# Kernel tuning notes

Hardware: AMD Instinct MI355X
Metric: run time of the kernel (lower is better)

## Reference

```python
import jax, jax.numpy as jnp
import numpy as np

NGF = 64
EPS = 1e-5


def _rpad(x):
    # ReflectionPad2d(1)
    return jnp.pad(x, ((0, 0), (0, 0), (1, 1), (1, 1)), mode='reflect')


def _inorm(x):
    # InstanceNorm2d(affine=False): per-sample, per-channel over H,W
    m = x.mean(axis=(2, 3), keepdims=True)
    v = ((x - m) ** 2).mean(axis=(2, 3), keepdims=True)
    return (x - m) / jnp.sqrt(v + EPS)


def _pac_conv(xp, gp, w, b):
    # Pixel-adaptive conv (pac.PacConv2d, kernel_type='gaussian', k=3, pad=0).
    # xp: (B,C,H+2,W+2) padded input; gp: (B,Cg,H+2,W+2) padded guide;
    # w: (O,C,3,3), b: (O,)
    B, C, Hp, Wp = xp.shape
    H, W = Hp - 2, Wp - 2
    gc = gp[:, :, 1:1 + H, 1:1 + W]  # guide value at each output pixel (patch center)
    out = jnp.zeros((B, w.shape[0], H, W), xp.dtype)
    for ky in range(3):
        for kx in range(3):
            gs = gp[:, :, ky:ky + H, kx:kx + W]
            # Gaussian adaptive kernel: exp(-0.5 * ||g_nb - g_center||^2), summed over guide channels
            k = jnp.exp(-0.5 * jnp.sum((gs - gc) ** 2, axis=1, keepdims=True))  # (B,1,H,W)
            xs = xp[:, :, ky:ky + H, kx:kx + W] * k
            out = out + jnp.einsum('oc,bchw->bohw', w[:, :, ky, kx], xs)
    return out + b[None, :, None, None]


def _pa_resblock(h, guide, wa, ba, wb, bb):
    gp = _rpad(guide)
    t = h
    h = _pac_conv(_rpad(h), gp, wa, ba)
    h = jax.nn.relu(_inorm(h))
    h = _pac_conv(_rpad(h), gp, wb, bb)
    h = _inorm(h)
    return t + h


def setup_inputs() -> dict:
    key = jax.random.key(0)
    ks = jax.random.split(key, 20)
    B, Cin, H, W = 4, 1, 256, 256
    d = {
        'x': jax.random.normal(ks[0], (B, Cin, H, W), jnp.float32),
        'grad_img': jax.random.normal(ks[1], (B, Cin, H, W), jnp.float32),
        'w0': jax.random.normal(ks[2], (NGF, Cin, 1, 1), jnp.float32) * 0.5,
        'b0': jnp.zeros((NGF,), jnp.float32),
        'wf': jax.random.normal(ks[3], (NGF, NGF, 3, 3), jnp.float32) * 0.05,
        'bf': jnp.zeros((NGF,), jnp.float32),
    }
    for i in (1, 2, 3):
        d[f'w{i}a'] = jax.random.normal(ks[3 + 2 * i], (NGF, NGF, 3, 3), jnp.float32) * 0.05
        d[f'b{i}a'] = jnp.zeros((NGF,), jnp.float32)
        d[f'w{i}b'] = jax.random.normal(ks[4 + 2 * i], (NGF, NGF, 3, 3), jnp.float32) * 0.05
        d[f'b{i}b'] = jnp.zeros((NGF,), jnp.float32)
    return d


def reference(x, grad_img, w0, b0, wf, bf,
              w1a, b1a, w1b, b1b,
              w2a, b2a, w2b, b2b,
              w3a, b3a, w3b, b3b):
    # type == 'ir': y = minmax(grad_img) is computed but unused; guide = x
    guide = x
    # 1x1 stem conv
    h = jnp.einsum('oc,bchw->bohw', w0[:, :, 0, 0], x) + b0[None, :, None, None]
    h = jax.nn.relu(_pa_resblock(h, guide, w1a, b1a, w1b, b1b))
    h = jax.nn.relu(_pa_resblock(h, guide, w2a, b2a, w2b, b2b))
    h = jax.nn.relu(_pa_resblock(h, guide, w3a, b3a, w3b, b3b))
    # model2: reflect pad + 3x3 conv + relu
    hp = _rpad(h)
    out = jax.lax.conv_general_dilated(
        hp, wf, window_strides=(1, 1), padding='VALID',
        dimension_numbers=('NCHW', 'OIHW', 'NCHW'))
    out = jax.nn.relu(out + bf[None, :, None, None])
    return out
```

## Files before the change

### kernel.cpp

```cpp
#include <hip/hip_runtime.h>
#include <hip/hip_bf16.h>
#include <math.h>

#define BN 4
#define CHN 64
#define HH 256
#define WW 256
#define HWSZ (HH*WW)
#define EPSV 1e-5f
#define CP 72

typedef __attribute__((ext_vector_type(8)))  short  short8;
typedef __attribute__((ext_vector_type(4)))  short  short4v;
typedef __attribute__((ext_vector_type(16))) float  floatx16;

__device__ __forceinline__ int refl(int i, int n){ if(i<0)i=-i; if(i>=n)i=2*n-2-i; return i; }
__device__ __forceinline__ short f2bf(float f){ __hip_bfloat16 h=__float2bfloat16(f); return __builtin_bit_cast(short,h); }
__device__ __forceinline__ float bf2f(short s){ unsigned u=((unsigned)(unsigned short)s)<<16; return __builtin_bit_cast(float,u); }

__global__ void guide_kernel(const float* __restrict__ x, float* __restrict__ Kb) {
    int idx = blockIdx.x * 256 + threadIdx.x;
    if (idx >= BN*HWSZ) return;
    int b = idx / HWSZ, p = idx - b*HWSZ;
    int y = p / WW, xx = p - y*WW;
    const float* g = x + b*HWSZ;
    float gc = g[p];
#pragma unroll
    for (int t = 0; t < 9; ++t) {
        int yy  = refl(y + t/3 - 1, HH);
        int xx2 = refl(xx + t%3 - 1, WW);
        float d = g[yy*WW + xx2] - gc;
        Kb[(b*9 + t)*HWSZ + p] = __expf(-0.5f*d*d);
    }
}

__global__ void pack_all(const float* w1,const float* w2,const float* w3,const float* w4,
                         const float* w5,const float* w6,const float* w7, short* __restrict__ Ap){
    const float* wsrc[7] = {w1,w2,w3,w4,w5,w6,w7};
    int layer = blockIdx.y;
    int tid = blockIdx.x*256 + threadIdx.x;
    int j    = tid & 7;
    int lane = (tid >> 3) & 63;
    int frag = tid >> 9;
    int oh = frag & 1, cg = (frag >> 1) & 3, t = frag >> 3;
    int o = oh*32 + (lane & 31);
    int c = cg*16 + (lane >> 5)*8 + j;
    Ap[(size_t)layer*36864 + tid] = f2bf(wsrc[layer][(o*CHN + c)*9 + t]);
}

__global__ void conv1x1_kernel(const float* __restrict__ x, const float* __restrict__ w0,
                               const float* __restrict__ b0, short* __restrict__ A){
    int idx = blockIdx.x*256 + threadIdx.x;
    int oc = idx & 7;
    int px = (idx >> 3) % HWSZ;
    int b  = idx / (HWSZ*8);
    float xv = x[(size_t)b*HWSZ + px];
    short8 r;
#pragma unroll
    for (int j = 0; j < 8; ++j) {
        int c = oc*8 + j;
        r[j] = f2bf(fmaf(w0[c], xv, b0[c]));
    }
    *(short8*)(A + ((size_t)(b*HWSZ + px))*64 + oc*8) = r;
}

__global__ void zero_stats(float* st){
    int idx = blockIdx.x*256 + threadIdx.x;
    if (idx < 6*BN*64*2) st[idx] = 0.f;
}

template<int NORM, int HASK, int FINAL>
__global__ void __launch_bounds__(256, 4) pac_mfma(
    const short* __restrict__ hin, const float* __restrict__ Kb,
    const short* __restrict__ Ap, const float* __restrict__ bias,
    const float* __restrict__ stin, short* __restrict__ outb, float* __restrict__ outf)
{
    __shared__ short lds[4*34*CP];

    int b  = blockIdx.z;
    int y0 = blockIdx.y * 2;
    int x0 = blockIdx.x * 32;
    int tid = threadIdx.x, lane = tid & 63, wave = tid >> 6;
    int ln2 = lane & 31, hi = lane >> 5, oh = wave & 1, wrow = wave >> 1;
    const short* hb = hin + (size_t)b*HWSZ*64;
    const float* stb = stin + b*64*2;

    float mean[8], rstd[8];
    if (NORM) {
        int c0 = (tid & 7) * 8;
#pragma unroll
        for (int j = 0; j < 8; ++j) {
            float s = stb[(c0+j)*2], s2 = stb[(c0+j)*2+1];
            float m = s * (1.f/HWSZ);
            float var = s2 * (1.f/HWSZ) - m*m;
            mean[j] = m; rstd[j] = rsqrtf(fmaxf(var, 0.f) + EPSV);
        }
    }
#pragma unroll
    for (int it = 0; it < 4; ++it) {
        int chunk = tid + it*256;
        int r = chunk >> 8, o = chunk & 255, px = o >> 3, oc = o & 7;
        int yy = refl(y0 - 1 + r, HH);
        short8 v = *(const short8*)(hb + ((size_t)(yy*WW + x0 + px))*64 + oc*8);
        if (NORM) {
#pragma unroll
            for (int j = 0; j < 8; ++j) {
                float f = bf2f(v[j]);
                f = fmaxf((f - mean[j]) * rstd[j], 0.f);
                v[j] = f2bf(f);
            }
        }
        *(short8*)(lds + (r*34 + 1 + px)*CP + oc*8) = v;
    }
    {
        int r = tid >> 6, c = tid & 63;
        int xm = (x0 == 0) ? 1 : x0 - 1;
        int xp = (x0 + 32 == WW) ? WW - 2 : x0 + 32;
        int yy = refl(y0 - 1 + r, HH);
        float fa = bf2f(hb[((size_t)(yy*WW + xm))*64 + c]);
        float fb = bf2f(hb[((size_t)(yy*WW + xp))*64 + c]);
        if (NORM) {
            float s = stb[c*2], s2 = stb[c*2+1];
            float m = s * (1.f/HWSZ);
            float rs = rsqrtf(fmaxf(s2*(1.f/HWSZ) - m*m, 0.f) + EPSV);
            fa = fmaxf((fa - m)*rs, 0.f);
            fb = fmaxf((fb - m)*rs, 0.f);
        }
        lds[(r*34 + 0)*CP + c]  = f2bf(fa);
        lds[(r*34 + 33)*CP + c] = f2bf(fb);
    }
    __syncthreads();

    float kv[9];
    if (HASK) {
#pragma unroll
        for (int t = 0; t < 9; ++t)
            kv[t] = Kb[((size_t)(b*9 + t))*HWSZ + (y0 + wrow)*WW + x0 + ln2];
    }

    floatx16 acc = (floatx16)(0.f);
    const short8* Ap8 = (const short8*)Ap;
#pragma unroll
    for (int t = 0; t < 9; ++t) {
        int dy = t/3 - 1, dx = t%3 - 1;
        int rr = wrow + dy + 1;
        floatx16 tmp;
#pragma unroll
        for (int cg = 0; cg < 4; ++cg) {
            short8 bf = *(const short8*)(lds + (rr*34 + 1 + ln2 + dx)*CP + cg*16 + hi*8);
            short8 af = Ap8[((size_t)(t*4 + cg)*2 + oh)*64 + lane];
            if (HASK)
                tmp = __builtin_amdgcn_mfma_f32_32x32x16_bf16(af, bf, cg == 0 ? (floatx16)(0.f) : tmp, 0, 0, 0);
            else
                acc = __builtin_amdgcn_mfma_f32_32x32x16_bf16(af, bf, acc, 0, 0, 0);
        }
        if (HASK) {
#pragma unroll
            for (int r = 0; r < 16; ++r) acc[r] = fmaf(kv[t], tmp[r], acc[r]);
        }
    }

    int y = y0 + wrow, x = x0 + ln2;
#pragma unroll
    for (int q = 0; q < 4; ++q) {
        int o0 = oh*32 + hi*4 + 8*q;
        float4 bq = *(const float4*)(bias + o0);
        if (FINAL) {
#pragma unroll
            for (int jj = 0; jj < 4; ++jj) {
                float val = acc[q*4 + jj] + ((float*)&bq)[jj];
                val = fmaxf(val, 0.f);
                outf[((size_t)(b*64 + o0 + jj))*HWSZ + y*WW + x] = val;
            }
        } else {
            short4v pk;
#pragma unroll
            for (int jj = 0; jj < 4; ++jj) pk[jj] = f2bf(acc[q*4 + jj] + ((float*)&bq)[jj]);
            *(short4v*)(outb + ((size_t)b*HWSZ + (size_t)(y*WW + x))*64 + o0) = pk;
        }
    }
}

__global__ void __launch_bounds__(256) stats_k(const short* __restrict__ t, float* __restrict__ st){
    int b = blockIdx.y, chunk = blockIdx.x;
    int tid = threadIdx.x, oc = tid & 7, pxl = tid >> 3;
    const short* tb = t + (size_t)b*HWSZ*64;
    float s[8] = {0}, s2[8] = {0};
    for (int i = 0; i < 64; ++i) {
        int px = chunk*2048 + i*32 + pxl;
        short8 v = *(const short8*)(tb + (size_t)px*64 + oc*8);
#pragma unroll
        for (int j = 0; j < 8; ++j) { float f = bf2f(v[j]); s[j] += f; s2[j] += f*f; }
    }
#pragma unroll
    for (int mask = 8; mask <= 32; mask <<= 1) {
#pragma unroll
        for (int j = 0; j < 8; ++j) { s[j] += __shfl_xor(s[j], mask); s2[j] += __shfl_xor(s2[j], mask); }
    }
    __shared__ float sm[4][8][16];
    int lane = tid & 63, wave = tid >> 6;
    if (lane < 8) {
#pragma unroll
        for (int j = 0; j < 8; ++j) { sm[wave][lane][j] = s[j]; sm[wave][lane][8+j] = s2[j]; }
    }
    __syncthreads();
    if (tid < 8) {
#pragma unroll
        for (int j = 0; j < 8; ++j) {
            float a = 0, bsq = 0;
#pragma unroll
            for (int w = 0; w < 4; ++w) { a += sm[w][tid][j]; bsq += sm[w][tid][8+j]; }
            atomicAdd(&st[(b*64 + tid*8 + j)*2],     a);
            atomicAdd(&st[(b*64 + tid*8 + j)*2 + 1], bsq);
        }
    }
}

__global__ void addnorm_relu(short* __restrict__ A, const short* __restrict__ C,
                             const float* __restrict__ st){
    int idx = blockIdx.x*256 + threadIdx.x;
    int oc = idx & 7;
    size_t pq = (size_t)(idx >> 3);
    int b = (int)(pq / HWSZ);
    size_t base = pq*64 + oc*8;
    short8 a = *(short8*)(A + base);
    short8 c = *(const short8*)(C + base);
#pragma unroll
    for (int j = 0; j < 8; ++j) {
        int cc = oc*8 + j;
        float s = st[(b*64+cc)*2], s2 = st[(b*64+cc)*2+1];
        float m = s * (1.f/HWSZ);
        float rs = rsqrtf(fmaxf(s2*(1.f/HWSZ) - m*m, 0.f) + EPSV);
        float f = bf2f(a[j]) + (bf2f(c[j]) - m)*rs;
        a[j] = f2bf(fmaxf(f, 0.f));
    }
    *(short8*)(A + base) = a;
}

extern "C" void kernel_launch(void* const* d_in, const int* in_sizes, int n_in,
                              void* d_out, int out_size, void* d_ws, size_t ws_size,
                              hipStream_t stream) {
    const float* x   = (const float*)d_in[0];
    const float* w0  = (const float*)d_in[2];
    const float* b0  = (const float*)d_in[3];
    const float* wf  = (const float*)d_in[4];
    const float* bf  = (const float*)d_in[5];
    const float* w1a = (const float*)d_in[6];  const float* b1a = (const float*)d_in[7];
    const float* w1b = (const float*)d_in[8];  const float* b1b = (const float*)d_in[9];
    const float* w2a = (const float*)d_in[10]; const float* b2a = (const float*)d_in[11];
    const float* w2b = (const float*)d_in[12]; const float* b2b = (const float*)d_in[13];
    const float* w3a = (const float*)d_in[14]; const float* b3a = (const float*)d_in[15];
    const float* w3b = (const float*)d_in[16]; const float* b3b = (const float*)d_in[17];

    float* ws   = (float*)d_ws;
    float* Kb   = ws;
    short* A    = (short*)(Kb + (size_t)BN*9*HWSZ);
    short* Bb   = A + (size_t)BN*HWSZ*64;
    short* Apk  = Bb + (size_t)BN*HWSZ*64;
    float* st   = (float*)(Apk + (size_t)7*36864 + 64);
    short* Cc   = (short*)d_out;

    zero_stats<<<12, 256, 0, stream>>>(st);
    pack_all<<<dim3(144, 7), 256, 0, stream>>>(w1a, w1b, w2a, w2b, w3a, w3b, wf, Apk);
    guide_kernel<<<(BN*HWSZ + 255)/256, 256, 0, stream>>>(x, Kb);
    conv1x1_kernel<<<BN*HWSZ*8/256, 256, 0, stream>>>(x, w0, b0, A);

    dim3 g(WW/32, HH/2, BN);
    const int eblk = BN*HWSZ*8/256;
    const float* biasA[3] = {b1a, b2a, b3a};
    const float* biasB[3] = {b1b, b2b, b3b};

    for (int rb = 0; rb < 3; ++rb) {
        float* stB = st + (size_t)(2*rb)   * BN*64*2;
        float* stC = st + (size_t)(2*rb+1) * BN*64*2;
        pac_mfma<0,1,0><<<g, 256, 0, stream>>>(A, Kb, Apk + (size_t)(2*rb)*36864, biasA[rb],
                                               nullptr, Bb, nullptr);
        stats_k<<<dim3(32, BN), 256, 0, stream>>>(Bb, stB);
        pac_mfma<1,1,0><<<g, 256, 0, stream>>>(Bb, Kb, Apk + (size_t)(2*rb+1)*36864, biasB[rb],
                                               stB, Cc, nullptr);
        stats_k<<<dim3(32, BN), 256, 0, stream>>>(Cc, stC);
        addnorm_relu<<<eblk, 256, 0, stream>>>(A, Cc, stC);
    }

    pac_mfma<0,0,1><<<g, 256, 0, stream>>>(A, Kb, Apk + (size_t)6*36864, bf,
                                           nullptr, nullptr, (float*)d_out);
}
```

Before: 545.4 us.

## Tile four output rows per block, each wave computing all 64 channels

The PAC MFMA kernel now covers four output rows per block instead of two, loading a 6-row halo into LDS through a unified loader that applies reflection on x. Each wave handles one row and both 32-channel output halves, reusing the B fragment across two MFMAs. This cuts the halo re-read overhead and the redundant LDS fragment loads. The stats kernel also gets twice as many blocks, each doing half the work, to raise parallelism. LDS use and register pressure per block go up, and the launch bound drops from 4 to 3 blocks per SM.

```diff
diff --git a/kernel.cpp b/kernel.cpp
--- a/kernel.cpp
+++ b/kernel.cpp
@@ -70,18 +70,18 @@
 }
 
 template<int NORM, int HASK, int FINAL>
-__global__ void __launch_bounds__(256, 4) pac_mfma(
+__global__ void __launch_bounds__(256, 3) pac_mfma(
     const short* __restrict__ hin, const float* __restrict__ Kb,
     const short* __restrict__ Ap, const float* __restrict__ bias,
     const float* __restrict__ stin, short* __restrict__ outb, float* __restrict__ outf)
 {
-    __shared__ short lds[4*34*CP];
+    __shared__ short lds[6*34*CP];
 
     int b  = blockIdx.z;
-    int y0 = blockIdx.y * 2;
+    int y0 = blockIdx.y * 4;
     int x0 = blockIdx.x * 32;
     int tid = threadIdx.x, lane = tid & 63, wave = tid >> 6;
-    int ln2 = lane & 31, hi = lane >> 5, oh = wave & 1, wrow = wave >> 1;
+    int ln2 = lane & 31, hi = lane >> 5;
     const short* hb = hin + (size_t)b*HWSZ*64;
     const float* stb = stin + b*64*2;
 
@@ -97,37 +97,25 @@
         }
     }
 #pragma unroll
-    for (int it = 0; it < 4; ++it) {
-        int chunk = tid + it*256;
-        int r = chunk >> 8, o = chunk & 255, px = o >> 3, oc = o & 7;
-        int yy = refl(y0 - 1 + r, HH);
-        short8 v = *(const short8*)(hb + ((size_t)(yy*WW + x0 + px))*64 + oc*8);
-        if (NORM) {
-#pragma unroll
-            for (int j = 0; j < 8; ++j) {
-                float f = bf2f(v[j]);
-                f = fmaxf((f - mean[j]) * rstd[j], 0.f);
-                v[j] = f2bf(f);
-            }
-        }
-        *(short8*)(lds + (r*34 + 1 + px)*CP + oc*8) = v;
-    }
-    {
-        int r = tid >> 6, c = tid & 63;
-        int xm = (x0 == 0) ? 1 : x0 - 1;
-        int xp = (x0 + 32 == WW) ? WW - 2 : x0 + 32;
-        int yy = refl(y0 - 1 + r, HH);
-        float fa = bf2f(hb[((size_t)(yy*WW + xm))*64 + c]);
-        float fb = bf2f(hb[((size_t)(yy*WW + xp))*64 + c]);
-        if (NORM) {
-            float s = stb[c*2], s2 = stb[c*2+1];
-            float m = s * (1.f/HWSZ);
-            float rs = rsqrtf(fmaxf(s2*(1.f/HWSZ) - m*m, 0.f) + EPSV);
-            fa = fmaxf((fa - m)*rs, 0.f);
-            fb = fmaxf((fb - m)*rs, 0.f);
-        }
-        lds[(r*34 + 0)*CP + c]  = f2bf(fa);
-        lds[(r*34 + 33)*CP + c] = f2bf(fb);
+    for (int it = 0; it < 7; ++it) {
+        int chunk = it*256 + tid;
+        if (chunk < 1632) {
+            int r = chunk / 272;
+            int rem = chunk - r*272;
+            int px = rem >> 3, oc = rem & 7;
+            int yy = refl(y0 - 1 + r, HH);
+            int xx = refl(x0 + px - 1, WW);
+            short8 v = *(const short8*)(hb + ((size_t)(yy*WW + xx))*64 + oc*8);
+            if (NORM) {
+#pragma unroll
+                for (int j = 0; j < 8; ++j) {
+                    float f = bf2f(v[j]);
+                    f = fmaxf((f - mean[j]) * rstd[j], 0.f);
+                    v[j] = f2bf(f);
+                }
+            }
+            *(short8*)(lds + (r*34 + px)*CP + oc*8) = v;
+        }
     }
     __syncthreads();
 
@@ -135,48 +123,58 @@
     if (HASK) {
 #pragma unroll
         for (int t = 0; t < 9; ++t)
-            kv[t] = Kb[((size_t)(b*9 + t))*HWSZ + (y0 + wrow)*WW + x0 + ln2];
-    }
-
-    floatx16 acc = (floatx16)(0.f);
+            kv[t] = Kb[((size_t)(b*9 + t))*HWSZ + (y0 + wave)*WW + x0 + ln2];
+    }
+
+    floatx16 acc[2] = {(floatx16)(0.f), (floatx16)(0.f)};
     const short8* Ap8 = (const short8*)Ap;
 #pragma unroll
     for (int t = 0; t < 9; ++t) {
         int dy = t/3 - 1, dx = t%3 - 1;
-        int rr = wrow + dy + 1;
-        floatx16 tmp;
+        int rr = wave + dy + 1;
+        floatx16 t0 = (floatx16)(0.f), t1 = (floatx16)(0.f);
 #pragma unroll
         for (int cg = 0; cg < 4; ++cg) {
-            short8 bf = *(const short8*)(lds + (rr*34 + 1 + ln2 + dx)*CP + cg*16 + hi*8);
-            short8 af = Ap8[((size_t)(t*4 + cg)*2 + oh)*64 + lane];
-            if (HASK)
-                tmp = __builtin_amdgcn_mfma_f32_32x32x16_bf16(af, bf, cg == 0 ? (floatx16)(0.f) : tmp, 0, 0, 0);
-            else
-                acc = __builtin_amdgcn_mfma_f32_32x32x16_bf16(af, bf, acc, 0, 0, 0);
+            short8 bf  = *(const short8*)(lds + (rr*34 + 1 + ln2 + dx)*CP + cg*16 + hi*8);
+            short8 af0 = Ap8[((size_t)(t*4 + cg)*2 + 0)*64 + lane];
+            short8 af1 = Ap8[((size_t)(t*4 + cg)*2 + 1)*64 + lane];
+            if (HASK) {
+                t0 = __builtin_amdgcn_mfma_f32_32x32x16_bf16(af0, bf, t0, 0, 0, 0);
+                t1 = __builtin_amdgcn_mfma_f32_32x32x16_bf16(af1, bf, t1, 0, 0, 0);
+            } else {
+                acc[0] = __builtin_amdgcn_mfma_f32_32x32x16_bf16(af0, bf, acc[0], 0, 0, 0);
+                acc[1] = __builtin_amdgcn_mfma_f32_32x32x16_bf16(af1, bf, acc[1], 0, 0, 0);
+            }
         }
         if (HASK) {
 #pragma unroll
-            for (int r = 0; r < 16; ++r) acc[r] = fmaf(kv[t], tmp[r], acc[r]);
-        }
-    }
-
-    int y = y0 + wrow, x = x0 + ln2;
-#pragma unroll
-    for (int q = 0; q < 4; ++q) {
-        int o0 = oh*32 + hi*4 + 8*q;
-        float4 bq = *(const float4*)(bias + o0);
-        if (FINAL) {
-#pragma unroll
-            for (int jj = 0; jj < 4; ++jj) {
-                float val = acc[q*4 + jj] + ((float*)&bq)[jj];
-                val = fmaxf(val, 0.f);
-                outf[((size_t)(b*64 + o0 + jj))*HWSZ + y*WW + x] = val;
-            }
-        } else {
-            short4v pk;
-#pragma unroll
-            for (int jj = 0; jj < 4; ++jj) pk[jj] = f2bf(acc[q*4 + jj] + ((float*)&bq)[jj]);
-            *(short4v*)(outb + ((size_t)b*HWSZ + (size_t)(y*WW + x))*64 + o0) = pk;
+            for (int r = 0; r < 16; ++r) {
+                acc[0][r] = fmaf(kv[t], t0[r], acc[0][r]);
+                acc[1][r] = fmaf(kv[t], t1[r], acc[1][r]);
+            }
+        }
+    }
+
+    int y = y0 + wave, x = x0 + ln2;
+#pragma unroll
+    for (int oh = 0; oh < 2; ++oh) {
+#pragma unroll
+        for (int q = 0; q < 4; ++q) {
+            int o0 = oh*32 + hi*4 + 8*q;
+            float4 bq = *(const float4*)(bias + o0);
+            if (FINAL) {
+#pragma unroll
+                for (int jj = 0; jj < 4; ++jj) {
+                    float val = acc[oh][q*4 + jj] + ((float*)&bq)[jj];
+                    val = fmaxf(val, 0.f);
+                    outf[((size_t)(b*64 + o0 + jj))*HWSZ + y*WW + x] = val;
+                }
+            } else {
+                short4v pk;
+#pragma unroll
+                for (int jj = 0; jj < 4; ++jj) pk[jj] = f2bf(acc[oh][q*4 + jj] + ((float*)&bq)[jj]);
+                *(short4v*)(outb + ((size_t)b*HWSZ + (size_t)(y*WW + x))*64 + o0) = pk;
+            }
         }
     }
 }
@@ -186,8 +184,8 @@
     int tid = threadIdx.x, oc = tid & 7, pxl = tid >> 3;
     const short* tb = t + (size_t)b*HWSZ*64;
     float s[8] = {0}, s2[8] = {0};
-    for (int i = 0; i < 64; ++i) {
-        int px = chunk*2048 + i*32 + pxl;
+    for (int i = 0; i < 32; ++i) {
+        int px = chunk*1024 + i*32 + pxl;
         short8 v = *(const short8*)(tb + (size_t)px*64 + oc*8);
 #pragma unroll
         for (int j = 0; j < 8; ++j) { float f = bf2f(v[j]); s[j] += f; s2[j] += f*f; }
@@ -265,7 +263,7 @@
     guide_kernel<<<(BN*HWSZ + 255)/256, 256, 0, stream>>>(x, Kb);
     conv1x1_kernel<<<BN*HWSZ*8/256, 256, 0, stream>>>(x, w0, b0, A);
 
-    dim3 g(WW/32, HH/2, BN);
+    dim3 g(WW/32, HH/4, BN);
     const int eblk = BN*HWSZ*8/256;
     const float* biasA[3] = {b1a, b2a, b3a};
     const float* biasB[3] = {b1b, b2b, b3b};
@@ -275,10 +273,10 @@
         float* stC = st + (size_t)(2*rb+1) * BN*64*2;
         pac_mfma<0,1,0><<<g, 256, 0, stream>>>(A, Kb, Apk + (size_t)(2*rb)*36864, biasA[rb],
                                                nullptr, Bb, nullptr);
-        stats_k<<<dim3(32, BN), 256, 0, stream>>>(Bb, stB);
+        stats_k<<<dim3(64, BN), 256, 0, stream>>>(Bb, stB);
         pac_mfma<1,1,0><<<g, 256, 0, stream>>>(Bb, Kb, Apk + (size_t)(2*rb+1)*36864, biasB[rb],
                                                stB, Cc, nullptr);
-        stats_k<<<dim3(32, BN), 256, 0, stream>>>(Cc, stC);
+        stats_k<<<dim3(64, BN), 256, 0, stream>>>(Cc, stC);
         addnorm_relu<<<eblk, 256, 0, stream>>>(A, Cc, stC);
     }
 
```

Result: slower. 701.2 us (+28.6%).

## Fuse instance-norm statistics into PAC conv epilogue and drop separate stats kernel

Applied to the files above, without the earlier changes.

Computes per-channel sum and sum-of-squares in the conv epilogue via wave shuffles, an LDS reduction and global atomics, removing the separate stats_k pass that re-read each 32MB bf16 intermediate. It also hoists the guide-kernel loads ahead of the LDS fill and batches the LDS and weight loads before the MFMA chain. Launch bounds are relaxed from 4 to 3 blocks per SM. In exchange there are many more atomics (one batch per block, over 16K blocks), extra shuffle work and register pressure, and possibly lower occupancy.

```diff
diff --git a/kernel.cpp b/kernel.cpp
--- a/kernel.cpp
+++ b/kernel.cpp
@@ -69,13 +69,15 @@
     if (idx < 6*BN*64*2) st[idx] = 0.f;
 }
 
-template<int NORM, int HASK, int FINAL>
-__global__ void __launch_bounds__(256, 4) pac_mfma(
+template<int NORM, int HASK, int FINAL, int STAT>
+__global__ void __launch_bounds__(256, 3) pac_mfma(
     const short* __restrict__ hin, const float* __restrict__ Kb,
     const short* __restrict__ Ap, const float* __restrict__ bias,
-    const float* __restrict__ stin, short* __restrict__ outb, float* __restrict__ outf)
+    const float* __restrict__ stin, short* __restrict__ outb, float* __restrict__ outf,
+    float* __restrict__ stout)
 {
     __shared__ short lds[4*34*CP];
+    __shared__ float sred[4][2][16][2];
 
     int b  = blockIdx.z;
     int y0 = blockIdx.y * 2;
@@ -84,6 +86,13 @@
     int ln2 = lane & 31, hi = lane >> 5, oh = wave & 1, wrow = wave >> 1;
     const short* hb = hin + (size_t)b*HWSZ*64;
     const float* stb = stin + b*64*2;
+
+    float kv[9];
+    if (HASK) {
+#pragma unroll
+        for (int t = 0; t < 9; ++t)
+            kv[t] = Kb[((size_t)(b*9 + t))*HWSZ + (y0 + wrow)*WW + x0 + ln2];
+    }
 
     float mean[8], rstd[8];
     if (NORM) {
@@ -131,36 +140,34 @@
     }
     __syncthreads();
 
-    float kv[9];
-    if (HASK) {
-#pragma unroll
-        for (int t = 0; t < 9; ++t)
-            kv[t] = Kb[((size_t)(b*9 + t))*HWSZ + (y0 + wrow)*WW + x0 + ln2];
-    }
-
     floatx16 acc = (floatx16)(0.f);
     const short8* Ap8 = (const short8*)Ap;
 #pragma unroll
     for (int t = 0; t < 9; ++t) {
         int dy = t/3 - 1, dx = t%3 - 1;
         int rr = wrow + dy + 1;
-        floatx16 tmp;
+        short8 bfr[4], af[4];
 #pragma unroll
         for (int cg = 0; cg < 4; ++cg) {
-            short8 bf = *(const short8*)(lds + (rr*34 + 1 + ln2 + dx)*CP + cg*16 + hi*8);
-            short8 af = Ap8[((size_t)(t*4 + cg)*2 + oh)*64 + lane];
-            if (HASK)
-                tmp = __builtin_amdgcn_mfma_f32_32x32x16_bf16(af, bf, cg == 0 ? (floatx16)(0.f) : tmp, 0, 0, 0);
-            else
-                acc = __builtin_amdgcn_mfma_f32_32x32x16_bf16(af, bf, acc, 0, 0, 0);
+            bfr[cg] = *(const short8*)(lds + (rr*34 + 1 + ln2 + dx)*CP + cg*16 + hi*8);
+            af[cg]  = Ap8[((size_t)(t*4 + cg)*2 + oh)*64 + lane];
         }
         if (HASK) {
+            floatx16 tmp = (floatx16)(0.f);
+#pragma unroll
+            for (int cg = 0; cg < 4; ++cg)
+                tmp = __builtin_amdgcn_mfma_f32_32x32x16_bf16(af[cg], bfr[cg], tmp, 0, 0, 0);
 #pragma unroll
             for (int r = 0; r < 16; ++r) acc[r] = fmaf(kv[t], tmp[r], acc[r]);
+        } else {
+#pragma unroll
+            for (int cg = 0; cg < 4; ++cg)
+                acc = __builtin_amdgcn_mfma_f32_32x32x16_bf16(af[cg], bfr[cg], acc, 0, 0, 0);
         }
     }
 
     int y = y0 + wrow, x = x0 + ln2;
+    float sv[16];
 #pragma unroll
     for (int q = 0; q < 4; ++q) {
         int o0 = oh*32 + hi*4 + 8*q;
@@ -175,43 +182,40 @@
         } else {
             short4v pk;
 #pragma unroll
-            for (int jj = 0; jj < 4; ++jj) pk[jj] = f2bf(acc[q*4 + jj] + ((float*)&bq)[jj]);
+            for (int jj = 0; jj < 4; ++jj) {
+                pk[jj] = f2bf(acc[q*4 + jj] + ((float*)&bq)[jj]);
+                sv[q*4 + jj] = bf2f(pk[jj]);
+            }
             *(short4v*)(outb + ((size_t)b*HWSZ + (size_t)(y*WW + x))*64 + o0) = pk;
         }
     }
-}
-
-__global__ void __launch_bounds__(256) stats_k(const short* __restrict__ t, float* __restrict__ st){
-    int b = blockIdx.y, chunk = blockIdx.x;
-    int tid = threadIdx.x, oc = tid & 7, pxl = tid >> 3;
-    const short* tb = t + (size_t)b*HWSZ*64;
-    float s[8] = {0}, s2[8] = {0};
-    for (int i = 0; i < 64; ++i) {
-        int px = chunk*2048 + i*32 + pxl;
-        short8 v = *(const short8*)(tb + (size_t)px*64 + oc*8);
-#pragma unroll
-        for (int j = 0; j < 8; ++j) { float f = bf2f(v[j]); s[j] += f; s2[j] += f*f; }
-    }
-#pragma unroll
-    for (int mask = 8; mask <= 32; mask <<= 1) {
-#pragma unroll
-        for (int j = 0; j < 8; ++j) { s[j] += __shfl_xor(s[j], mask); s2[j] += __shfl_xor(s2[j], mask); }
-    }
-    __shared__ float sm[4][8][16];
-    int lane = tid & 63, wave = tid >> 6;
-    if (lane < 8) {
-#pragma unroll
-        for (int j = 0; j < 8; ++j) { sm[wave][lane][j] = s[j]; sm[wave][lane][8+j] = s2[j]; }
-    }
-    __syncthreads();
-    if (tid < 8) {
-#pragma unroll
-        for (int j = 0; j < 8; ++j) {
-            float a = 0, bsq = 0;
-#pragma unroll
-            for (int w = 0; w < 4; ++w) { a += sm[w][tid][j]; bsq += sm[w][tid][8+j]; }
-            atomicAdd(&st[(b*64 + tid*8 + j)*2],     a);
-            atomicAdd(&st[(b*64 + tid*8 + j)*2 + 1], bsq);
+
+    if (STAT) {
+        float s1[16], s2[16];
+#pragma unroll
+        for (int r = 0; r < 16; ++r) { s1[r] = sv[r]; s2[r] = sv[r]*sv[r]; }
+#pragma unroll
+        for (int mask = 1; mask < 32; mask <<= 1) {
+#pragma unroll
+            for (int r = 0; r < 16; ++r) {
+                s1[r] += __shfl_xor(s1[r], mask);
+                s2[r] += __shfl_xor(s2[r], mask);
+            }
+        }
+        if (ln2 == 0) {
+#pragma unroll
+            for (int r = 0; r < 16; ++r) {
+                sred[wave][hi][r][0] = s1[r];
+                sred[wave][hi][r][1] = s2[r];
+            }
+        }
+        __syncthreads();
+        if (tid < 128) {
+            int reg = tid & 15, hh = (tid >> 4) & 1, ohh = (tid >> 5) & 1, stat = tid >> 6;
+            float v = sred[ohh][hh][reg][stat] + sred[ohh + 2][hh][reg][stat];
+            int q = reg >> 2, jj = reg & 3;
+            int c = ohh*32 + hh*4 + 8*q + jj;
+            atomicAdd(&stout[(b*64 + c)*2 + stat], v);
         }
     }
 }
@@ -273,15 +277,13 @@
     for (int rb = 0; rb < 3; ++rb) {
         float* stB = st + (size_t)(2*rb)   * BN*64*2;
         float* stC = st + (size_t)(2*rb+1) * BN*64*2;
-        pac_mfma<0,1,0><<<g, 256, 0, stream>>>(A, Kb, Apk + (size_t)(2*rb)*36864, biasA[rb],
-                                               nullptr, Bb, nullptr);
-        stats_k<<<dim3(32, BN), 256, 0, stream>>>(Bb, stB);
-        pac_mfma<1,1,0><<<g, 256, 0, stream>>>(Bb, Kb, Apk + (size_t)(2*rb+1)*36864, biasB[rb],
-                                               stB, Cc, nullptr);
-        stats_k<<<dim3(32, BN), 256, 0, stream>>>(Cc, stC);
+        pac_mfma<0,1,0,1><<<g, 256, 0, stream>>>(A, Kb, Apk + (size_t)(2*rb)*36864, biasA[rb],
+                                                 nullptr, Bb, nullptr, stB);
+        pac_mfma<1,1,0,1><<<g, 256, 0, stream>>>(Bb, Kb, Apk + (size_t)(2*rb+1)*36864, biasB[rb],
+                                                 stB, Cc, nullptr, stC);
         addnorm_relu<<<eblk, 256, 0, stream>>>(A, Cc, stC);
     }
 
-    pac_mfma<0,0,1><<<g, 256, 0, stream>>>(A, Kb, Apk + (size_t)6*36864, bf,
-                                           nullptr, nullptr, (float*)d_out);
-}
+    pac_mfma<0,0,1,0><<<g, 256, 0, stream>>>(A, Kb, Apk + (size_t)6*36864, bf,
+                                             nullptr, nullptr, (float*)d_out, nullptr);
+}
```

Result: slower. 1.011 ms (+85.3%).

## Fuse residual add-norm into next PAC conv and software-pipeline MFMA operand loads

Applied to the files above, without the earlier changes.

The residual add + instance-norm + ReLU of the first two resblocks moves into the load stage of the next block's first PAC conv (MODE 2). That kernel writes the fused activation to a scratch buffer for the following residual, which removes two standalone elementwise passes over the full activation tensor. The MFMA loop now prefetches the next tap's LDS and weight fragments, splits the per-tap accumulation into two independent MFMA chains, and uses packed float2 FMAs. Launch bounds drop to 2 blocks per SM to allow more registers, and stats_k uses twice as many blocks. Lower occupancy and extra global reads of the C tensor in halo regions are the tradeoffs, and the scratch buffer is placed past the output in d_out.

```diff
diff --git a/kernel.cpp b/kernel.cpp
--- a/kernel.cpp
+++ b/kernel.cpp
@@ -12,6 +12,7 @@
 
 typedef __attribute__((ext_vector_type(8)))  short  short8;
 typedef __attribute__((ext_vector_type(4)))  short  short4v;
+typedef __attribute__((ext_vector_type(2)))  float  float2v;
 typedef __attribute__((ext_vector_type(16))) float  floatx16;
 
 __device__ __forceinline__ int refl(int i, int n){ if(i<0)i=-i; if(i>=n)i=2*n-2-i; return i; }
@@ -69,11 +70,13 @@
     if (idx < 6*BN*64*2) st[idx] = 0.f;
 }
 
-template<int NORM, int HASK, int FINAL>
-__global__ void __launch_bounds__(256, 4) pac_mfma(
-    const short* __restrict__ hin, const float* __restrict__ Kb,
+template<int MODE, int HASK, int FINAL, int WRITES>
+__global__ void __launch_bounds__(256, 2) pac_mfma(
+    const short* __restrict__ hin, const short* __restrict__ cin,
+    const float* __restrict__ Kb,
     const short* __restrict__ Ap, const float* __restrict__ bias,
-    const float* __restrict__ stin, short* __restrict__ outb, float* __restrict__ outf)
+    const float* __restrict__ stin, short* __restrict__ outb, float* __restrict__ outf,
+    short* __restrict__ snew)
 {
     __shared__ short lds[4*34*CP];
 
@@ -83,10 +86,23 @@
     int tid = threadIdx.x, lane = tid & 63, wave = tid >> 6;
     int ln2 = lane & 31, hi = lane >> 5, oh = wave & 1, wrow = wave >> 1;
     const short* hb = hin + (size_t)b*HWSZ*64;
-    const float* stb = stin + b*64*2;
+    const short* cb = (MODE == 2) ? cin + (size_t)b*HWSZ*64 : nullptr;
+    const float* stb = (MODE >= 1) ? stin + b*64*2 : nullptr;
+
+    float kv[9];
+    if (HASK) {
+#pragma unroll
+        for (int t = 0; t < 9; ++t)
+            kv[t] = Kb[((size_t)(b*9 + t))*HWSZ + (y0 + wrow)*WW + x0 + ln2];
+    }
+    const short8* Ap8 = (const short8*)Ap;
+    short8 acur[4];
+#pragma unroll
+    for (int cg = 0; cg < 4; ++cg)
+        acur[cg] = Ap8[((size_t)(0*4 + cg)*2 + oh)*64 + lane];
 
     float mean[8], rstd[8];
-    if (NORM) {
+    if (MODE >= 1) {
         int c0 = (tid & 7) * 8;
 #pragma unroll
         for (int j = 0; j < 8; ++j) {
@@ -101,14 +117,19 @@
         int chunk = tid + it*256;
         int r = chunk >> 8, o = chunk & 255, px = o >> 3, oc = o & 7;
         int yy = refl(y0 - 1 + r, HH);
-        short8 v = *(const short8*)(hb + ((size_t)(yy*WW + x0 + px))*64 + oc*8);
-        if (NORM) {
-#pragma unroll
-            for (int j = 0; j < 8; ++j) {
-                float f = bf2f(v[j]);
-                f = fmaxf((f - mean[j]) * rstd[j], 0.f);
-                v[j] = f2bf(f);
-            }
+        size_t base = ((size_t)(yy*WW + x0 + px))*64 + oc*8;
+        short8 v = *(const short8*)(hb + base);
+        if (MODE == 1) {
+#pragma unroll
+            for (int j = 0; j < 8; ++j)
+                v[j] = f2bf(fmaxf((bf2f(v[j]) - mean[j]) * rstd[j], 0.f));
+        } else if (MODE == 2) {
+            short8 c = *(const short8*)(cb + base);
+#pragma unroll
+            for (int j = 0; j < 8; ++j)
+                v[j] = f2bf(fmaxf(bf2f(v[j]) + (bf2f(c[j]) - mean[j]) * rstd[j], 0.f));
+            if (WRITES && (r == 1 || r == 2))
+                *(short8*)(snew + (size_t)b*HWSZ*64 + base) = v;
         }
         *(short8*)(lds + (r*34 + 1 + px)*CP + oc*8) = v;
     }
@@ -117,47 +138,65 @@
         int xm = (x0 == 0) ? 1 : x0 - 1;
         int xp = (x0 + 32 == WW) ? WW - 2 : x0 + 32;
         int yy = refl(y0 - 1 + r, HH);
-        float fa = bf2f(hb[((size_t)(yy*WW + xm))*64 + c]);
-        float fb = bf2f(hb[((size_t)(yy*WW + xp))*64 + c]);
-        if (NORM) {
+        size_t ba = ((size_t)(yy*WW + xm))*64 + c;
+        size_t bb2 = ((size_t)(yy*WW + xp))*64 + c;
+        float fa = bf2f(hb[ba]), fb = bf2f(hb[bb2]);
+        if (MODE >= 1) {
             float s = stb[c*2], s2 = stb[c*2+1];
             float m = s * (1.f/HWSZ);
             float rs = rsqrtf(fmaxf(s2*(1.f/HWSZ) - m*m, 0.f) + EPSV);
-            fa = fmaxf((fa - m)*rs, 0.f);
-            fb = fmaxf((fb - m)*rs, 0.f);
+            if (MODE == 1) {
+                fa = fmaxf((fa - m)*rs, 0.f);
+                fb = fmaxf((fb - m)*rs, 0.f);
+            } else {
+                fa = fmaxf(fa + (bf2f(cb[ba])  - m)*rs, 0.f);
+                fb = fmaxf(fb + (bf2f(cb[bb2]) - m)*rs, 0.f);
+            }
         }
         lds[(r*34 + 0)*CP + c]  = f2bf(fa);
         lds[(r*34 + 33)*CP + c] = f2bf(fb);
     }
     __syncthreads();
 
-    float kv[9];
-    if (HASK) {
-#pragma unroll
-        for (int t = 0; t < 9; ++t)
-            kv[t] = Kb[((size_t)(b*9 + t))*HWSZ + (y0 + wrow)*WW + x0 + ln2];
-    }
-
     floatx16 acc = (floatx16)(0.f);
-    const short8* Ap8 = (const short8*)Ap;
+    short8 bcur[4];
+#pragma unroll
+    for (int cg = 0; cg < 4; ++cg)
+        bcur[cg] = *(const short8*)(lds + (wrow*34 + ln2)*CP + cg*16 + hi*8);
+
 #pragma unroll
     for (int t = 0; t < 9; ++t) {
-        int dy = t/3 - 1, dx = t%3 - 1;
-        int rr = wrow + dy + 1;
-        floatx16 tmp;
-#pragma unroll
-        for (int cg = 0; cg < 4; ++cg) {
-            short8 bf = *(const short8*)(lds + (rr*34 + 1 + ln2 + dx)*CP + cg*16 + hi*8);
-            short8 af = Ap8[((size_t)(t*4 + cg)*2 + oh)*64 + lane];
-            if (HASK)
-                tmp = __builtin_amdgcn_mfma_f32_32x32x16_bf16(af, bf, cg == 0 ? (floatx16)(0.f) : tmp, 0, 0, 0);
-            else
-                acc = __builtin_amdgcn_mfma_f32_32x32x16_bf16(af, bf, acc, 0, 0, 0);
+        short8 bnx[4], anx[4];
+        if (t < 8) {
+            int tn = t + 1, dy = tn/3 - 1, dx = tn%3 - 1;
+            int rr = wrow + dy + 1;
+#pragma unroll
+            for (int cg = 0; cg < 4; ++cg) {
+                bnx[cg] = *(const short8*)(lds + (rr*34 + 1 + ln2 + dx)*CP + cg*16 + hi*8);
+                anx[cg] = Ap8[((size_t)(tn*4 + cg)*2 + oh)*64 + lane];
+            }
         }
         if (HASK) {
-#pragma unroll
-            for (int r = 0; r < 16; ++r) acc[r] = fmaf(kv[t], tmp[r], acc[r]);
-        }
+            floatx16 t0 = (floatx16)(0.f), t1 = (floatx16)(0.f);
+            t0 = __builtin_amdgcn_mfma_f32_32x32x16_bf16(acur[0], bcur[0], t0, 0, 0, 0);
+            t1 = __builtin_amdgcn_mfma_f32_32x32x16_bf16(acur[2], bcur[2], t1, 0, 0, 0);
+            t0 = __builtin_amdgcn_mfma_f32_32x32x16_bf16(acur[1], bcur[1], t0, 0, 0, 0);
+            t1 = __builtin_amdgcn_mfma_f32_32x32x16_bf16(acur[3], bcur[3], t1, 0, 0, 0);
+            float2v kv2 = {kv[t], kv[t]};
+            float2v* a2 = (float2v*)&acc;
+            float2v* p0 = (float2v*)&t0;
+            float2v* p1 = (float2v*)&t1;
+#pragma unroll
+            for (int r = 0; r < 8; ++r) a2[r] = __builtin_elementwise_fma(kv2, p0[r], a2[r]);
+#pragma unroll
+            for (int r = 0; r < 8; ++r) a2[r] = __builtin_elementwise_fma(kv2, p1[r], a2[r]);
+        } else {
+#pragma unroll
+            for (int cg = 0; cg < 4; ++cg)
+                acc = __builtin_amdgcn_mfma_f32_32x32x16_bf16(acur[cg], bcur[cg], acc, 0, 0, 0);
+        }
+#pragma unroll
+        for (int cg = 0; cg < 4; ++cg) { bcur[cg] = bnx[cg]; acur[cg] = anx[cg]; }
     }
 
     int y = y0 + wrow, x = x0 + ln2;
@@ -175,7 +214,8 @@
         } else {
             short4v pk;
 #pragma unroll
-            for (int jj = 0; jj < 4; ++jj) pk[jj] = f2bf(acc[q*4 + jj] + ((float*)&bq)[jj]);
+            for (int jj = 0; jj < 4; ++jj)
+                pk[jj] = f2bf(acc[q*4 + jj] + ((float*)&bq)[jj]);
             *(short4v*)(outb + ((size_t)b*HWSZ + (size_t)(y*WW + x))*64 + o0) = pk;
         }
     }
@@ -186,8 +226,8 @@
     int tid = threadIdx.x, oc = tid & 7, pxl = tid >> 3;
     const short* tb = t + (size_t)b*HWSZ*64;
     float s[8] = {0}, s2[8] = {0};
-    for (int i = 0; i < 64; ++i) {
-        int px = chunk*2048 + i*32 + pxl;
+    for (int i = 0; i < 32; ++i) {
+        int px = chunk*1024 + i*32 + pxl;
         short8 v = *(const short8*)(tb + (size_t)px*64 + oc*8);
 #pragma unroll
         for (int j = 0; j < 8; ++j) { float f = bf2f(v[j]); s[j] += f; s2[j] += f*f; }
@@ -216,25 +256,25 @@
     }
 }
 
-__global__ void addnorm_relu(short* __restrict__ A, const short* __restrict__ C,
-                             const float* __restrict__ st){
+__global__ void addnorm_relu(short* __restrict__ dst, const short* __restrict__ a,
+                             const short* __restrict__ c, const float* __restrict__ st){
     int idx = blockIdx.x*256 + threadIdx.x;
     int oc = idx & 7;
     size_t pq = (size_t)(idx >> 3);
     int b = (int)(pq / HWSZ);
     size_t base = pq*64 + oc*8;
-    short8 a = *(short8*)(A + base);
-    short8 c = *(const short8*)(C + base);
+    short8 av = *(const short8*)(a + base);
+    short8 cv = *(const short8*)(c + base);
 #pragma unroll
     for (int j = 0; j < 8; ++j) {
         int cc = oc*8 + j;
         float s = st[(b*64+cc)*2], s2 = st[(b*64+cc)*2+1];
         float m = s * (1.f/HWSZ);
         float rs = rsqrtf(fmaxf(s2*(1.f/HWSZ) - m*m, 0.f) + EPSV);
-        float f = bf2f(a[j]) + (bf2f(c[j]) - m)*rs;
-        a[j] = f2bf(fmaxf(f, 0.f));
-    }
-    *(short8*)(A + base) = a;
+        float f = bf2f(av[j]) + (bf2f(cv[j]) - m)*rs;
+        av[j] = f2bf(fmaxf(f, 0.f));
+    }
+    *(short8*)(dst + base) = av;
 }
 
 extern "C" void kernel_launch(void* const* d_in, const int* in_sizes, int n_in,
@@ -259,6 +299,7 @@
     short* Apk  = Bb + (size_t)BN*HWSZ*64;
     float* st   = (float*)(Apk + (size_t)7*36864 + 64);
     short* Cc   = (short*)d_out;
+    short* Sp   = Cc + (size_t)BN*HWSZ*64;
 
     zero_stats<<<12, 256, 0, stream>>>(st);
     pack_all<<<dim3(144, 7), 256, 0, stream>>>(w1a, w1b, w2a, w2b, w3a, w3b, wf, Apk);
@@ -267,21 +308,22 @@
 
     dim3 g(WW/32, HH/2, BN);
     const int eblk = BN*HWSZ*8/256;
-    const float* biasA[3] = {b1a, b2a, b3a};
-    const float* biasB[3] = {b1b, b2b, b3b};
-
-    for (int rb = 0; rb < 3; ++rb) {
-        float* stB = st + (size_t)(2*rb)   * BN*64*2;
-        float* stC = st + (size_t)(2*rb+1) * BN*64*2;
-        pac_mfma<0,1,0><<<g, 256, 0, stream>>>(A, Kb, Apk + (size_t)(2*rb)*36864, biasA[rb],
-                                               nullptr, Bb, nullptr);
-        stats_k<<<dim3(32, BN), 256, 0, stream>>>(Bb, stB);
-        pac_mfma<1,1,0><<<g, 256, 0, stream>>>(Bb, Kb, Apk + (size_t)(2*rb+1)*36864, biasB[rb],
-                                               stB, Cc, nullptr);
-        stats_k<<<dim3(32, BN), 256, 0, stream>>>(Cc, stC);
-        addnorm_relu<<<eblk, 256, 0, stream>>>(A, Cc, stC);
-    }
-
-    pac_mfma<0,0,1><<<g, 256, 0, stream>>>(A, Kb, Apk + (size_t)6*36864, bf,
-                                           nullptr, nullptr, (float*)d_out);
-}
+    float* st1 = st;            float* stc1 = st + 512;
+    float* st2 = st + 1024;     float* stc2 = st + 1536;
+    float* st3 = st + 2048;     float* stc3 = st + 2560;
+
+    pac_mfma<0,1,0,0><<<g,256,0,stream>>>(A,  nullptr, Kb, Apk,            b1a, nullptr, Bb, nullptr, nullptr);
+    stats_k<<<dim3(64,BN),256,0,stream>>>(Bb, st1);
+    pac_mfma<1,1,0,0><<<g,256,0,stream>>>(Bb, nullptr, Kb, Apk + 36864,    b1b, st1,     Cc, nullptr, nullptr);
+    stats_k<<<dim3(64,BN),256,0,stream>>>(Cc, stc1);
+    pac_mfma<2,1,0,1><<<g,256,0,stream>>>(A,  Cc,      Kb, Apk + 2*36864,  b2a, stc1,    Bb, nullptr, Sp);
+    stats_k<<<dim3(64,BN),256,0,stream>>>(Bb, st2);
+    pac_mfma<1,1,0,0><<<g,256,0,stream>>>(Bb, nullptr, Kb, Apk + 3*36864,  b2b, st2,     Cc, nullptr, nullptr);
+    stats_k<<<dim3(64,BN),256,0,stream>>>(Cc, stc2);
+    pac_mfma<2,1,0,1><<<g,256,0,stream>>>(Sp, Cc,      Kb, Apk + 4*36864,  b3a, stc2,    Bb, nullptr, A);
+    stats_k<<<dim3(64,BN),256,0,stream>>>(Bb, st3);
+    pac_mfma<1,1,0,0><<<g,256,0,stream>>>(Bb, nullptr, Kb, Apk + 5*36864,  b3b, st3,     Cc, nullptr, nullptr);
+    stats_k<<<dim3(64,BN),256,0,stream>>>(Cc, stc3);
+    addnorm_relu<<<eblk,256,0,stream>>>(Bb, A, Cc, stc3);
+    pac_mfma<0,0,1,0><<<g,256,0,stream>>>(Bb, nullptr, Kb, Apk + 6*36864,  bf,  nullptr, nullptr, (float*)d_out, nullptr);
+}
```

New measurement: 609.2 us. +11.7%, slower.
